# Optimization experiments

Hardware: AMD Instinct MI355X
Metric: run time of the kernel (lower is better)

The kernel has to match this reference:

```python
import jax, jax.numpy as jnp
import numpy as np

B, C, N, CIN, COUT, ORDER = 16, 32, 207, 64, 64, 2
SCALE = COUT / (ORDER * CIN)          # = 0.5
BN_EVAL = 1.0 / np.sqrt(1.0 + 1e-5)   # eval-mode BatchNorm2d at init (mean=0, var=1)


def setup_inputs() -> dict:
    key = jax.random.key(0)
    ks = jax.random.split(key, 9)
    s = 0.05  # xavier-ish small init scale
    return {
        "x":          jax.random.normal(ks[0], (B, C, N, CIN), dtype=jnp.float32),
        "res_weight": jax.random.normal(ks[1], (C, N, CIN, COUT, ORDER), dtype=jnp.float32) * s,
        "res_bias":   jax.random.normal(ks[2], (1, C, N, 1, 1), dtype=jnp.float32) * s,
        "mlp_w":      jax.random.normal(ks[3], (COUT, CIN), dtype=jnp.float32) * s,
        "mlp_b":      jax.random.normal(ks[4], (COUT,), dtype=jnp.float32) * s,
        "gate_w":     jax.random.normal(ks[5], (COUT, CIN), dtype=jnp.float32) * s,
        "gate_b":     jax.random.normal(ks[6], (COUT,), dtype=jnp.float32) * s,
        "order_w":    jax.random.normal(ks[7], (ORDER,), dtype=jnp.float32) * s,
        "order_b":    jax.random.normal(ks[8], (1,), dtype=jnp.float32) * s,
    }


def reference(x, res_weight, res_bias, mlp_w, mlp_b, gate_w, gate_b, order_w, order_b):
    # shared linear branch (dropout = identity in eval)
    x_share = jnp.einsum('bcni,oi->bcno', x, mlp_w) + mlp_b            # [B,C,N,COUT]
    # polynomial features: h[..., 0]=x, h[..., 1]=BN(x*x) (eval BN ~ identity scale)
    x1 = (x * x) * BN_EVAL
    h = jnp.stack([x, x1], axis=-1)                                    # [B,C,N,CIN,ORDER]
    # per-(channel,node) grouped linear
    x_uniq = jnp.einsum('bcnid,cniod->bcnod', h, res_weight) + res_bias  # [B,C,N,COUT,ORDER]
    # order_mlp: Linear(order -> 1), squeeze
    x_uniq = jnp.einsum('bcnod,d->bcno', x_uniq, order_w) + order_b    # [B,C,N,COUT]
    x_uniq = x_uniq * (SCALE / 4.0)
    # sigmoid gate combine + residual
    gate = jax.nn.sigmoid(jnp.einsum('bcni,oi->bcno', x, gate_w) + gate_b)
    return gate * x_uniq + (1.0 - gate) * x_share + x
```

## Files before the change

kernel.cpp:

```cpp
#include <hip/hip_runtime.h>
#include <math.h>

#define Bdim 16
#define Cdim 32
#define Ndim 207
#define CINd 64
#define COUTd 64

#define X_B (Cdim * Ndim * CINd)
#define X_C (Ndim * CINd)
#define W_C (Ndim * CINd * COUTd * 2)
#define W_N (CINd * COUTd * 2)

#define BN_EVAL 0.9999950000374997f

__global__ __launch_bounds__(256, 4)
void fused_multilinear(const float* __restrict__ x,
                       const float* __restrict__ rw,
                       const float* __restrict__ rb,
                       const float* __restrict__ mw,
                       const float* __restrict__ mb,
                       const float* __restrict__ gw,
                       const float* __restrict__ gb,
                       const float* __restrict__ ow,
                       const float* __restrict__ obp,
                       float* __restrict__ out)
{
    __shared__ float2 mg[64 * 65];

    const int cn = blockIdx.x;
    const int c  = cn / Ndim;
    const int n  = cn % Ndim;
    const int o  = threadIdx.x & 63;
    const int bg = __builtin_amdgcn_readfirstlane((int)(threadIdx.x >> 6));

    for (int t = threadIdx.x; t < 4096; t += 256) {
        const int oo = t >> 6;
        const int ii = t & 63;
        mg[ii * 65 + oo] = make_float2(mw[t], gw[t]);
    }
    __syncthreads();

    const float* wbase = rw + (size_t)c * W_C + (size_t)n * W_N + (size_t)(o * 2);
    const float* xb0   = x + (size_t)c * X_C + (size_t)(n * CINd);

    const float* xr[4];
#pragma unroll
    for (int j = 0; j < 4; ++j)
        xr[j] = xb0 + (size_t)(bg * 4 + j) * X_B;

    float acc0[4] = {0.f, 0.f, 0.f, 0.f};
    float acc1[4] = {0.f, 0.f, 0.f, 0.f};
    float accS[4] = {0.f, 0.f, 0.f, 0.f};
    float accG[4] = {0.f, 0.f, 0.f, 0.f};

    for (int i0 = 0; i0 < 64; i0 += 8) {
        float xv[4][8];
#pragma unroll
        for (int j = 0; j < 4; ++j) {
            const float4 a  = *(const float4*)(xr[j] + i0);
            const float4 b4 = *(const float4*)(xr[j] + i0 + 4);
            xv[j][0] = a.x;  xv[j][1] = a.y;  xv[j][2] = a.z;  xv[j][3] = a.w;
            xv[j][4] = b4.x; xv[j][5] = b4.y; xv[j][6] = b4.z; xv[j][7] = b4.w;
        }
#pragma unroll
        for (int k = 0; k < 8; ++k) {
            const int i = i0 + k;
            const float2 w = *(const float2*)(wbase + (size_t)i * 128);
            const float2 m = mg[i * 65 + o];
#pragma unroll
            for (int j = 0; j < 4; ++j) {
                const float xb = xv[j][k];
                acc0[j] = __builtin_fmaf(xb, w.x, acc0[j]);
                const float t = xb * w.y;
                acc1[j] = __builtin_fmaf(xb, t, acc1[j]);
                accS[j] = __builtin_fmaf(xb, m.x, accS[j]);
                accG[j] = __builtin_fmaf(xb, m.y, accG[j]);
            }
        }
    }

    const float rbias = rb[c * Ndim + n];
    const float ow0 = ow[0], ow1 = ow[1], obias = obp[0];
    const float mbias = mb[o];
    const float gbias = gb[o];

#pragma unroll
    for (int j = 0; j < 4; ++j) {
        const int b = bg * 4 + j;
        float uniq = (acc0[j] + rbias) * ow0
                   + (BN_EVAL * acc1[j] + rbias) * ow1
                   + obias;
        uniq *= 0.125f;

        const float xs = accS[j] + mbias;
        const float zg = accG[j] + gbias;
        const float g  = 1.0f / (1.0f + __expf(-zg));

        const size_t idx = (size_t)b * X_B + (size_t)c * X_C + (size_t)(n * CINd) + o;
        out[idx] = g * uniq + (1.0f - g) * xs + x[idx];
    }
}

extern "C" void kernel_launch(void* const* d_in, const int* in_sizes, int n_in,
                              void* d_out, int out_size, void* d_ws, size_t ws_size,
                              hipStream_t stream)
{
    const float* x   = (const float*)d_in[0];
    const float* rw  = (const float*)d_in[1];
    const float* rb  = (const float*)d_in[2];
    const float* mw  = (const float*)d_in[3];
    const float* mb  = (const float*)d_in[4];
    const float* gw  = (const float*)d_in[5];
    const float* gb  = (const float*)d_in[6];
    const float* ow  = (const float*)d_in[7];
    const float* ob  = (const float*)d_in[8];
    float* out = (float*)d_out;

    fused_multilinear<<<dim3(Cdim * Ndim), dim3(256), 0, stream>>>(
        x, rw, rb, mw, mb, gw, gb, ow, ob, out);
}
```

Before: 378.6 us.

## Double-buffer weight and x loads and use packed float2 FMAs

Fully unrolls the CIN loop and prefetches the next chunk of residual weights and x values into registers while the current chunk is computed. The accumulators become 2-wide vectors so the compiler can emit packed FP32 FMA instructions. The shared-memory padding for the mlp/gate weights is removed, since each lane reads consecutive float2 entries anyway. This raises register pressure under the 4-blocks-per-CU launch bound, which could cause spills or lower occupancy in a memory-bound kernel.

```diff
diff --git a/kernel.cpp b/kernel.cpp
--- a/kernel.cpp
+++ b/kernel.cpp
@@ -14,6 +14,8 @@
 
 #define BN_EVAL 0.9999950000374997f
 
+typedef float v2f __attribute__((ext_vector_type(2)));
+
 __global__ __launch_bounds__(256, 4)
 void fused_multilinear(const float* __restrict__ x,
                        const float* __restrict__ rw,
@@ -26,7 +28,7 @@
                        const float* __restrict__ obp,
                        float* __restrict__ out)
 {
-    __shared__ float2 mg[64 * 65];
+    __shared__ float2 mg[64 * 64];
 
     const int cn = blockIdx.x;
     const int c  = cn / Ndim;
@@ -37,7 +39,7 @@
     for (int t = threadIdx.x; t < 4096; t += 256) {
         const int oo = t >> 6;
         const int ii = t & 63;
-        mg[ii * 65 + oo] = make_float2(mw[t], gw[t]);
+        mg[ii * 64 + oo] = make_float2(mw[t], gw[t]);
     }
     __syncthreads();
 
@@ -49,33 +51,66 @@
     for (int j = 0; j < 4; ++j)
         xr[j] = xb0 + (size_t)(bg * 4 + j) * X_B;
 
-    float acc0[4] = {0.f, 0.f, 0.f, 0.f};
-    float acc1[4] = {0.f, 0.f, 0.f, 0.f};
-    float accS[4] = {0.f, 0.f, 0.f, 0.f};
-    float accG[4] = {0.f, 0.f, 0.f, 0.f};
+    v2f acc01[4];
+    v2f accSG[4];
+#pragma unroll
+    for (int j = 0; j < 4; ++j) { acc01[j] = (v2f)(0.f); accSG[j] = (v2f)(0.f); }
 
-    for (int i0 = 0; i0 < 64; i0 += 8) {
-        float xv[4][8];
+    float2 wcur[8], wnxt[8];
+    float4 xcur[4][2], xnxt[4][2];
+
 #pragma unroll
-        for (int j = 0; j < 4; ++j) {
-            const float4 a  = *(const float4*)(xr[j] + i0);
-            const float4 b4 = *(const float4*)(xr[j] + i0 + 4);
-            xv[j][0] = a.x;  xv[j][1] = a.y;  xv[j][2] = a.z;  xv[j][3] = a.w;
-            xv[j][4] = b4.x; xv[j][5] = b4.y; xv[j][6] = b4.z; xv[j][7] = b4.w;
+    for (int k = 0; k < 8; ++k)
+        wcur[k] = *(const float2*)(wbase + (size_t)k * 128);
+#pragma unroll
+    for (int j = 0; j < 4; ++j) {
+        xcur[j][0] = *(const float4*)(xr[j] + 0);
+        xcur[j][1] = *(const float4*)(xr[j] + 4);
+    }
+
+#pragma unroll
+    for (int c8 = 0; c8 < 8; ++c8) {
+        const int i0 = c8 * 8;
+
+        if (c8 < 7) {
+            const int i1 = i0 + 8;
+#pragma unroll
+            for (int k = 0; k < 8; ++k)
+                wnxt[k] = *(const float2*)(wbase + (size_t)(i1 + k) * 128);
+#pragma unroll
+            for (int j = 0; j < 4; ++j) {
+                xnxt[j][0] = *(const float4*)(xr[j] + i1);
+                xnxt[j][1] = *(const float4*)(xr[j] + i1 + 4);
+            }
         }
+
 #pragma unroll
         for (int k = 0; k < 8; ++k) {
             const int i = i0 + k;
-            const float2 w = *(const float2*)(wbase + (size_t)i * 128);
-            const float2 m = mg[i * 65 + o];
+            const v2f wv = { wcur[k].x, wcur[k].y };
+            const float2 mraw = mg[i * 64 + o];
+            const v2f mv = { mraw.x, mraw.y };
+            const float4 a = xcur[0][k >> 2];
 #pragma unroll
             for (int j = 0; j < 4; ++j) {
-                const float xb = xv[j][k];
-                acc0[j] = __builtin_fmaf(xb, w.x, acc0[j]);
-                const float t = xb * w.y;
-                acc1[j] = __builtin_fmaf(xb, t, acc1[j]);
-                accS[j] = __builtin_fmaf(xb, m.x, accS[j]);
-                accG[j] = __builtin_fmaf(xb, m.y, accG[j]);
+                const float4 q = xcur[j][k >> 2];
+                const float xb = (k & 3) == 0 ? q.x : (k & 3) == 1 ? q.y
+                               : (k & 3) == 2 ? q.z : q.w;
+                const v2f xx  = { xb, xb * xb };
+                acc01[j] += xx * wv;
+                const v2f xbb = { xb, xb };
+                accSG[j] += xbb * mv;
+            }
+            (void)a;
+        }
+
+        if (c8 < 7) {
+#pragma unroll
+            for (int k = 0; k < 8; ++k) wcur[k] = wnxt[k];
+#pragma unroll
+            for (int j = 0; j < 4; ++j) {
+                xcur[j][0] = xnxt[j][0];
+                xcur[j][1] = xnxt[j][1];
             }
         }
     }
@@ -88,13 +123,13 @@
 #pragma unroll
     for (int j = 0; j < 4; ++j) {
         const int b = bg * 4 + j;
-        float uniq = (acc0[j] + rbias) * ow0
-                   + (BN_EVAL * acc1[j] + rbias) * ow1
+        float uniq = (acc01[j].x + rbias) * ow0
+                   + (BN_EVAL * acc01[j].y + rbias) * ow1
                    + obias;
         uniq *= 0.125f;
 
-        const float xs = accS[j] + mbias;
-        const float zg = accG[j] + gbias;
+        const float xs = accSG[j].x + mbias;
+        const float zg = accSG[j].y + gbias;
         const float g  = 1.0f / (1.0f + __expf(-zg));
 
         const size_t idx = (size_t)b * X_B + (size_t)c * X_C + (size_t)(n * CINd) + o;
```

After: 445.9 us. 17.8% more time.

## Double-buffer res_weight chunks into LDS via async global_load_lds and pack FMAs

Applied to the files above, without the earlier changes.

The per-(c,n) weight tile is now streamed in 16-row chunks directly from global memory into a double-buffered LDS region with global_load_lds, prefetching the next chunk while the current one is consumed. This is meant to hide the global-memory latency of the weight reads that dominated the loop. The accumulators are also packed into 2-wide vectors so the compiler can emit packed FMAs. The cost is extra LDS use, a block-wide barrier per chunk and a lower occupancy hint in the launch bounds (4 down to 3).

```diff
diff --git a/kernel.cpp b/kernel.cpp
--- a/kernel.cpp
+++ b/kernel.cpp
@@ -14,7 +14,20 @@
 
 #define BN_EVAL 0.9999950000374997f
 
-__global__ __launch_bounds__(256, 4)
+#define CHUNK_I      16
+#define CHUNK_FLOATS (CHUNK_I * COUTd * 2)
+#define NCHUNK       4
+
+typedef float v2f __attribute__((ext_vector_type(2)));
+
+__device__ __forceinline__ void dma16(const float* g, float* lds) {
+    __builtin_amdgcn_global_load_lds(
+        (const __attribute__((address_space(1))) unsigned int*)g,
+        (__attribute__((address_space(3))) unsigned int*)lds,
+        16, 0, 0);
+}
+
+__global__ __launch_bounds__(256, 3)
 void fused_multilinear(const float* __restrict__ x,
                        const float* __restrict__ rw,
                        const float* __restrict__ rb,
@@ -27,12 +40,27 @@
                        float* __restrict__ out)
 {
     __shared__ float2 mg[64 * 65];
+    __shared__ float rwbuf[2][CHUNK_FLOATS];
 
     const int cn = blockIdx.x;
     const int c  = cn / Ndim;
     const int n  = cn % Ndim;
     const int o  = threadIdx.x & 63;
-    const int bg = __builtin_amdgcn_readfirstlane((int)(threadIdx.x >> 6));
+    const int wvid = __builtin_amdgcn_readfirstlane((int)(threadIdx.x >> 6));
+
+    const float* wtile = rw + (size_t)c * W_C + (size_t)n * W_N;
+    const float* xb0   = x + (size_t)c * X_C + (size_t)(n * CINd);
+
+    const float* xr[4];
+#pragma unroll
+    for (int j = 0; j < 4; ++j)
+        xr[j] = xb0 + (size_t)(wvid * 4 + j) * X_B;
+
+    {
+        const float* g = wtile + wvid * 512 + o * 4;
+        dma16(g,       &rwbuf[0][wvid * 512]);
+        dma16(g + 256, &rwbuf[0][wvid * 512 + 256]);
+    }
 
     for (int t = threadIdx.x; t < 4096; t += 256) {
         const int oo = t >> 6;
@@ -41,43 +69,47 @@
     }
     __syncthreads();
 
-    const float* wbase = rw + (size_t)c * W_C + (size_t)n * W_N + (size_t)(o * 2);
-    const float* xb0   = x + (size_t)c * X_C + (size_t)(n * CINd);
+    v2f acc01[4];
+    v2f accSG[4];
+#pragma unroll
+    for (int j = 0; j < 4; ++j) { acc01[j] = (v2f)(0.f); accSG[j] = (v2f)(0.f); }
 
-    const float* xr[4];
+    for (int cc = 0; cc < NCHUNK; ++cc) {
+        const int p = cc & 1;
+
+        if (cc < NCHUNK - 1) {
+            const float* g = wtile + (cc + 1) * CHUNK_FLOATS + wvid * 512 + o * 4;
+            dma16(g,       &rwbuf[p ^ 1][wvid * 512]);
+            dma16(g + 256, &rwbuf[p ^ 1][wvid * 512 + 256]);
+        }
+
+        float4 xq[4][4];
 #pragma unroll
-    for (int j = 0; j < 4; ++j)
-        xr[j] = xb0 + (size_t)(bg * 4 + j) * X_B;
+        for (int j = 0; j < 4; ++j)
+#pragma unroll
+            for (int q = 0; q < 4; ++q)
+                xq[j][q] = *(const float4*)(xr[j] + cc * CHUNK_I + q * 4);
 
-    float acc0[4] = {0.f, 0.f, 0.f, 0.f};
-    float acc1[4] = {0.f, 0.f, 0.f, 0.f};
-    float accS[4] = {0.f, 0.f, 0.f, 0.f};
-    float accG[4] = {0.f, 0.f, 0.f, 0.f};
-
-    for (int i0 = 0; i0 < 64; i0 += 8) {
-        float xv[4][8];
 #pragma unroll
-        for (int j = 0; j < 4; ++j) {
-            const float4 a  = *(const float4*)(xr[j] + i0);
-            const float4 b4 = *(const float4*)(xr[j] + i0 + 4);
-            xv[j][0] = a.x;  xv[j][1] = a.y;  xv[j][2] = a.z;  xv[j][3] = a.w;
-            xv[j][4] = b4.x; xv[j][5] = b4.y; xv[j][6] = b4.z; xv[j][7] = b4.w;
-        }
-#pragma unroll
-        for (int k = 0; k < 8; ++k) {
-            const int i = i0 + k;
-            const float2 w = *(const float2*)(wbase + (size_t)i * 128);
-            const float2 m = mg[i * 65 + o];
+        for (int k = 0; k < CHUNK_I; ++k) {
+            const int i = cc * CHUNK_I + k;
+            const float2 w2 = *(const float2*)&rwbuf[p][k * 128 + o * 2];
+            const v2f wv = { w2.x, w2.y };
+            const float2 m2 = mg[i * 65 + o];
+            const v2f mv = { m2.x, m2.y };
 #pragma unroll
             for (int j = 0; j < 4; ++j) {
-                const float xb = xv[j][k];
-                acc0[j] = __builtin_fmaf(xb, w.x, acc0[j]);
-                const float t = xb * w.y;
-                acc1[j] = __builtin_fmaf(xb, t, acc1[j]);
-                accS[j] = __builtin_fmaf(xb, m.x, accS[j]);
-                accG[j] = __builtin_fmaf(xb, m.y, accG[j]);
+                const float4 q4 = xq[j][k >> 2];
+                const float xb = (k & 3) == 0 ? q4.x : (k & 3) == 1 ? q4.y
+                               : (k & 3) == 2 ? q4.z : q4.w;
+                const v2f xx  = { xb, xb * xb };
+                acc01[j] += xx * wv;
+                const v2f xbb = { xb, xb };
+                accSG[j] += xbb * mv;
             }
         }
+
+        __syncthreads();
     }
 
     const float rbias = rb[c * Ndim + n];
@@ -87,14 +119,14 @@
 
 #pragma unroll
     for (int j = 0; j < 4; ++j) {
-        const int b = bg * 4 + j;
-        float uniq = (acc0[j] + rbias) * ow0
-                   + (BN_EVAL * acc1[j] + rbias) * ow1
+        const int b = wvid * 4 + j;
+        float uniq = (acc01[j].x + rbias) * ow0
+                   + (BN_EVAL * acc01[j].y + rbias) * ow1
                    + obias;
         uniq *= 0.125f;
 
-        const float xs = accS[j] + mbias;
-        const float zg = accG[j] + gbias;
+        const float xs = accSG[j].x + mbias;
+        const float zg = accSG[j].y + gbias;
         const float g  = 1.0f / (1.0f + __expf(-zg));
 
         const size_t idx = (size_t)b * X_B + (size_t)c * X_C + (size_t)(n * CINd) + o;
```

After: 457.5 us. 20.8% more time.

## Compute grouped, shared and gate linears with bf16 MFMA instructions

Applied to the files above, without the earlier changes.

Replaces the scalar FMA loops with bf16 16x16x32 MFMA. The polynomial features (x*ow0, x^2*BN*ow1) are interleaved in LDS so the grouped weight and the order mix collapse into one K=128 product. The shared and gate weights are converted to bf16 in LDS and multiplied against bf16 x. This cuts the VALU work and issues all weight loads up front, at the cost of bf16 rounding on activations and weights.

```diff
diff --git a/kernel.cpp b/kernel.cpp
--- a/kernel.cpp
+++ b/kernel.cpp
@@ -1,104 +1,120 @@
 #include <hip/hip_runtime.h>
-#include <math.h>
 
 #define Bdim 16
 #define Cdim 32
 #define Ndim 207
-#define CINd 64
-#define COUTd 64
-
-#define X_B (Cdim * Ndim * CINd)
-#define X_C (Ndim * CINd)
-#define W_C (Ndim * CINd * COUTd * 2)
-#define W_N (CINd * COUTd * 2)
-
+#define X_B (Cdim * Ndim * 64)
+#define X_C (Ndim * 64)
+#define W_C (Ndim * 64 * 64 * 2)
+#define W_N (64 * 64 * 2)
 #define BN_EVAL 0.9999950000374997f
 
+using s8v = __attribute__((ext_vector_type(8))) short;
+using f4v = __attribute__((ext_vector_type(4))) float;
+
+union UV { uint4 u; s8v s; };
+
+__device__ __forceinline__ unsigned pk(float lo, float hi) {
+    union { float f; unsigned u; } a, b;
+    a.f = lo; b.f = hi;
+    return __builtin_amdgcn_perm(b.u, a.u, 0x07060302u);
+}
+
 __global__ __launch_bounds__(256, 4)
-void fused_multilinear(const float* __restrict__ x,
-                       const float* __restrict__ rw,
-                       const float* __restrict__ rb,
-                       const float* __restrict__ mw,
-                       const float* __restrict__ mb,
-                       const float* __restrict__ gw,
-                       const float* __restrict__ gb,
-                       const float* __restrict__ ow,
-                       const float* __restrict__ obp,
-                       float* __restrict__ out)
+void fused_ml_mfma(const float* __restrict__ x,
+                   const float* __restrict__ rw,
+                   const float* __restrict__ rb,
+                   const float* __restrict__ mw,
+                   const float* __restrict__ mb,
+                   const float* __restrict__ gw,
+                   const float* __restrict__ gb,
+                   const float* __restrict__ ow,
+                   const float* __restrict__ obp,
+                   float* __restrict__ out)
 {
-    __shared__ float2 mg[64 * 65];
+    __shared__ unsigned short A1[16 * 136];
+    __shared__ unsigned short A2[16 * 72];
+    __shared__ unsigned short MG[128 * 72];
 
-    const int cn = blockIdx.x;
-    const int c  = cn / Ndim;
-    const int n  = cn % Ndim;
-    const int o  = threadIdx.x & 63;
-    const int bg = __builtin_amdgcn_readfirstlane((int)(threadIdx.x >> 6));
+    const int cn = blockIdx.x, c = cn / Ndim, n = cn % Ndim;
+    const int t = threadIdx.x;
+    const float ow0 = ow[0], ow1 = ow[1];
+    const float bnow1 = ow1 * BN_EVAL;
 
-    for (int t = threadIdx.x; t < 4096; t += 256) {
-        const int oo = t >> 6;
-        const int ii = t & 63;
-        mg[ii * 65 + oo] = make_float2(mw[t], gw[t]);
+    {
+        const int b = t >> 4, i0 = (t & 15) * 4;
+        const float* xrow = x + (size_t)b * X_B + (size_t)c * X_C + n * 64;
+        const float4 xv = *(const float4*)(xrow + i0);
+        uint4 v;
+        v.x = pk(xv.x * ow0, xv.x * xv.x * bnow1);
+        v.y = pk(xv.y * ow0, xv.y * xv.y * bnow1);
+        v.z = pk(xv.z * ow0, xv.z * xv.z * bnow1);
+        v.w = pk(xv.w * ow0, xv.w * xv.w * bnow1);
+        *(uint4*)&A1[b * 136 + i0 * 2] = v;
+        uint2 p;
+        p.x = pk(xv.x, xv.y);
+        p.y = pk(xv.z, xv.w);
+        *(uint2*)&A2[b * 72 + i0] = p;
+    }
+    {
+        const int r = t >> 1, h = t & 1;
+        const float* src = (r < 64 ? mw + r * 64 : gw + (r - 64) * 64) + h * 32;
+        unsigned short* dst = &MG[r * 72 + h * 32];
+#pragma unroll
+        for (int u = 0; u < 4; ++u) {
+            const float4 a4 = ((const float4*)src)[2 * u];
+            const float4 b4 = ((const float4*)src)[2 * u + 1];
+            uint4 v;
+            v.x = pk(a4.x, a4.y); v.y = pk(a4.z, a4.w);
+            v.z = pk(b4.x, b4.y); v.w = pk(b4.z, b4.w);
+            *(uint4*)&dst[u * 8] = v;
+        }
     }
     __syncthreads();
 
-    const float* wbase = rw + (size_t)c * W_C + (size_t)n * W_N + (size_t)(o * 2);
-    const float* xb0   = x + (size_t)c * X_C + (size_t)(n * CINd);
+    const int l = t & 63, w = t >> 6, q = l >> 4, nn = l & 15;
+    const int o = w * 16 + nn;
+    const float* wtile = rw + (size_t)c * W_C + (size_t)n * W_N + o * 2;
 
-    const float* xr[4];
+    f4v accU = {0.f, 0.f, 0.f, 0.f};
+    f4v accM = {0.f, 0.f, 0.f, 0.f};
+    f4v accG = {0.f, 0.f, 0.f, 0.f};
+
 #pragma unroll
-    for (int j = 0; j < 4; ++j)
-        xr[j] = xb0 + (size_t)(bg * 4 + j) * X_B;
-
-    float acc0[4] = {0.f, 0.f, 0.f, 0.f};
-    float acc1[4] = {0.f, 0.f, 0.f, 0.f};
-    float accS[4] = {0.f, 0.f, 0.f, 0.f};
-    float accG[4] = {0.f, 0.f, 0.f, 0.f};
-
-    for (int i0 = 0; i0 < 64; i0 += 8) {
-        float xv[4][8];
+    for (int s = 0; s < 4; ++s) {
+        const float* gp = wtile + (size_t)(16 * s + 4 * q) * 128;
+        const float2 w0 = *(const float2*)(gp);
+        const float2 w1 = *(const float2*)(gp + 128);
+        const float2 w2 = *(const float2*)(gp + 256);
+        const float2 w3 = *(const float2*)(gp + 384);
+        UV bu;
+        bu.u.x = pk(w0.x, w0.y); bu.u.y = pk(w1.x, w1.y);
+        bu.u.z = pk(w2.x, w2.y); bu.u.w = pk(w3.x, w3.y);
+        UV au; au.u = *(const uint4*)&A1[nn * 136 + 32 * s + 8 * q];
+        accU = __builtin_amdgcn_mfma_f32_16x16x32_bf16(au.s, bu.s, accU, 0, 0, 0);
+    }
 #pragma unroll
-        for (int j = 0; j < 4; ++j) {
-            const float4 a  = *(const float4*)(xr[j] + i0);
-            const float4 b4 = *(const float4*)(xr[j] + i0 + 4);
-            xv[j][0] = a.x;  xv[j][1] = a.y;  xv[j][2] = a.z;  xv[j][3] = a.w;
-            xv[j][4] = b4.x; xv[j][5] = b4.y; xv[j][6] = b4.z; xv[j][7] = b4.w;
-        }
-#pragma unroll
-        for (int k = 0; k < 8; ++k) {
-            const int i = i0 + k;
-            const float2 w = *(const float2*)(wbase + (size_t)i * 128);
-            const float2 m = mg[i * 65 + o];
-#pragma unroll
-            for (int j = 0; j < 4; ++j) {
-                const float xb = xv[j][k];
-                acc0[j] = __builtin_fmaf(xb, w.x, acc0[j]);
-                const float t = xb * w.y;
-                acc1[j] = __builtin_fmaf(xb, t, acc1[j]);
-                accS[j] = __builtin_fmaf(xb, m.x, accS[j]);
-                accG[j] = __builtin_fmaf(xb, m.y, accG[j]);
-            }
-        }
+    for (int s = 0; s < 2; ++s) {
+        UV a2u; a2u.u = *(const uint4*)&A2[nn * 72 + 32 * s + 8 * q];
+        UV bm;  bm.u  = *(const uint4*)&MG[o * 72 + 32 * s + 8 * q];
+        UV bg2; bg2.u = *(const uint4*)&MG[(64 + o) * 72 + 32 * s + 8 * q];
+        accM = __builtin_amdgcn_mfma_f32_16x16x32_bf16(a2u.s, bm.s,  accM, 0, 0, 0);
+        accG = __builtin_amdgcn_mfma_f32_16x16x32_bf16(a2u.s, bg2.s, accG, 0, 0, 0);
     }
 
     const float rbias = rb[c * Ndim + n];
-    const float ow0 = ow[0], ow1 = ow[1], obias = obp[0];
-    const float mbias = mb[o];
-    const float gbias = gb[o];
-
+    const float uconst = rbias * (ow0 + ow1) + obp[0];
+    const float mbias = mb[o], gbias = gb[o];
+    const float* xcol = x + (size_t)c * X_C + n * 64 + o;
+    float* ocol = out + (size_t)c * X_C + n * 64 + o;
 #pragma unroll
-    for (int j = 0; j < 4; ++j) {
-        const int b = bg * 4 + j;
-        float uniq = (acc0[j] + rbias) * ow0
-                   + (BN_EVAL * acc1[j] + rbias) * ow1
-                   + obias;
-        uniq *= 0.125f;
-
-        const float xs = accS[j] + mbias;
-        const float zg = accG[j] + gbias;
-        const float g  = 1.0f / (1.0f + __expf(-zg));
-
-        const size_t idx = (size_t)b * X_B + (size_t)c * X_C + (size_t)(n * CINd) + o;
-        out[idx] = g * uniq + (1.0f - g) * xs + x[idx];
+    for (int r = 0; r < 4; ++r) {
+        const int b = q * 4 + r;
+        const float uniq = (accU[r] + uconst) * 0.125f;
+        const float xs = accM[r] + mbias;
+        const float g = 1.f / (1.f + __expf(-(accG[r] + gbias)));
+        const float xres = xcol[(size_t)b * X_B];
+        ocol[(size_t)b * X_B] = g * uniq + (1.f - g) * xs + xres;
     }
 }
 
@@ -117,6 +133,6 @@
     const float* ob  = (const float*)d_in[8];
     float* out = (float*)d_out;
 
-    fused_multilinear<<<dim3(Cdim * Ndim), dim3(256), 0, stream>>>(
+    fused_ml_mfma<<<dim3(Cdim * Ndim), dim3(256), 0, stream>>>(
         x, rw, rb, mw, mb, gw, gb, ow, ob, out);
 }
```

Result: faster. 334.9 us (-11.5%).
